# Kernel tuning notes

Hardware: AMD Instinct MI355X
Metric: run time of the kernel (lower is better)

Reference implementation:

```python
import jax, jax.numpy as jnp
import numpy as np

N_NODES = 50000
N_EDGES = 800000
D_FEAT = 128
UNITS = 128


def setup_inputs() -> dict:
    key = jax.random.key(0)
    k1, k2, k3, k4 = jax.random.split(key, 4)
    x = jax.random.normal(k1, (N_NODES, D_FEAT), dtype=jnp.float32)
    source = jax.random.randint(k2, (N_EDGES,), 0, N_NODES, dtype=jnp.int32)
    target = jax.random.randint(k3, (N_EDGES,), 0, N_NODES, dtype=jnp.int32)
    W = jax.random.normal(k4, (D_FEAT, UNITS), dtype=jnp.float32) * (1.0 / np.sqrt(D_FEAT))
    b = jnp.zeros((UNITS,), dtype=jnp.float32)
    return {"x": x, "source": source, "target": target, "W": W, "b": b}


def _degree(idx, n_nodes):
    # in/out degree = segment-sum of unit edge weights; clamp to >= 1 (no self loops)
    deg = jnp.zeros((n_nodes,), dtype=jnp.float32).at[idx].add(1.0)
    return jnp.maximum(deg, 1.0)


def reference(x, source, target, W, b):
    n = x.shape[0]
    # degree_normalization == "in_out": sender scale from out-degree, receiver from in-degree
    sender_scale = jax.lax.rsqrt(_degree(source, n))[:, None]      # [N, 1]
    receiver_scale = jax.lax.rsqrt(_degree(target, n))[:, None]    # [N, 1]
    normalized = sender_scale * x                                  # [N, D]
    source_bcast = normalized[source]                              # [E, D] gather
    pooled = jax.ops.segment_sum(source_bcast, target, num_segments=n)  # [N, D] scatter-add
    pooled = receiver_scale * pooled
    # Dense(units, activation='relu', use_bias=True)
    return jax.nn.relu(pooled @ W + b)
```

## Files before the change

### kernel.cpp

```cpp
#include <hip/hip_runtime.h>
#include <hip/hip_bf16.h>

#define N_FEAT 128
#define EPT 8
#define CHUNK 2048
#define BSHIFT 8
#define MAXRANGE 256
#define CAP 8192
#define LSTR 66

typedef short bf16x8 __attribute__((ext_vector_type(8)));
typedef float f32x4  __attribute__((ext_vector_type(4)));

__device__ __forceinline__ unsigned short f2bf_rtne(float f) {
    unsigned u = __float_as_uint(f);
    u += 0x7fffu + ((u >> 16) & 1u);
    return (unsigned short)(u >> 16);
}
__device__ __forceinline__ float bf2f(unsigned short h) {
    return __uint_as_float((unsigned)h << 16);
}

__global__ __launch_bounds__(256) void scatter_kernel(const int* __restrict__ source,
                                                      const int* __restrict__ target,
                                                      int* __restrict__ curT,
                                                      int* __restrict__ curS,
                                                      unsigned int* __restrict__ pairsT,
                                                      unsigned char* __restrict__ srcB,
                                                      const float* __restrict__ W,
                                                      unsigned short* __restrict__ Whi,
                                                      unsigned short* __restrict__ Wlo,
                                                      int E, int NB, int NBLK) {
    __shared__ unsigned int   lds_pairs[CHUNK];
    __shared__ unsigned short lds_sp[CHUNK];
    __shared__ int ct[MAXRANGE], cs[MAXRANGE];
    __shared__ int st[MAXRANGE], ss[MAXRANGE];
    __shared__ int gt[MAXRANGE], gs[MAXRANGE];
    int tid = threadIdx.x, b = blockIdx.x;

    if (b >= NBLK) {
        int idx = (b - NBLK) * 256 + tid;
        int lane = idx & 63;
        int ks = (idx >> 6) & 3;
        int ct2 = idx >> 8;
        int n  = ct2 * 16 + (lane & 15);
        int k0 = ks * 32 + (lane >> 4) * 8;
        unsigned short h[8], l[8];
        #pragma unroll
        for (int j = 0; j < 8; ++j) {
            float w = W[(k0 + j) * N_FEAT + n];
            unsigned short hh = f2bf_rtne(w);
            h[j] = hh;
            l[j] = f2bf_rtne(w - bf2f(hh));
        }
        size_t off = (size_t)idx * 8;
        *(ushort4*)(Whi + off)     = make_ushort4(h[0], h[1], h[2], h[3]);
        *(ushort4*)(Whi + off + 4) = make_ushort4(h[4], h[5], h[6], h[7]);
        *(ushort4*)(Wlo + off)     = make_ushort4(l[0], l[1], l[2], l[3]);
        *(ushort4*)(Wlo + off + 4) = make_ushort4(l[4], l[5], l[6], l[7]);
        return;
    }

    int base = b * CHUNK;
    int cnt = E - base; if (cnt > CHUNK) cnt = CHUNK;

    int rs[EPT], rt[EPT];
    ct[tid] = 0; cs[tid] = 0;
    __syncthreads();
    #pragma unroll
    for (int j = 0; j < EPT; ++j) {
        int e = base + j * 256 + tid;
        if (e < E) {
            int s = source[e], t = target[e];
            rs[j] = s; rt[j] = t;
            atomicAdd(&ct[t >> BSHIFT], 1);
            atomicAdd(&cs[s >> BSHIFT], 1);
        }
    }
    __syncthreads();
    int vt = ct[tid], vs = cs[tid];
    st[tid] = vt; ss[tid] = vs;
    __syncthreads();
    #pragma unroll
    for (int off = 1; off < 256; off <<= 1) {
        int t1 = (tid >= off) ? st[tid - off] : 0;
        int t2 = (tid >= off) ? ss[tid - off] : 0;
        __syncthreads();
        st[tid] += t1; ss[tid] += t2;
        __syncthreads();
    }
    int et = st[tid] - vt, es = ss[tid] - vs;
    int gT = 0, gS = 0;
    if (tid < NB) {
        if (vt) gT = atomicAdd(&curT[tid], vt);
        if (vs) gS = atomicAdd(&curS[tid], vs);
    }
    __syncthreads();
    st[tid] = et; ss[tid] = es;
    ct[tid] = et; cs[tid] = es;
    gt[tid] = gT; gs[tid] = gS;
    __syncthreads();
    #pragma unroll
    for (int j = 0; j < EPT; ++j) {
        int e = base + j * 256 + tid;
        if (e < E) {
            int s = rs[j], t = rt[j];
            int k = t >> BSHIFT;
            int p = atomicAdd(&ct[k], 1);
            lds_pairs[p] = (unsigned)s | ((unsigned)t << 16);
            int k2 = s >> BSHIFT;
            int p2 = atomicAdd(&cs[k2], 1);
            lds_sp[p2] = (unsigned short)s;
        }
    }
    __syncthreads();
    for (int i = tid; i < cnt; i += 256) {
        unsigned w = lds_pairs[i];
        int k = w >> 24;
        pairsT[(size_t)k * CAP + gt[k] + (i - st[k])] = w;
        unsigned short sp = lds_sp[i];
        int k2 = sp >> 8;
        srcB[(size_t)k2 * CAP + gs[k2] + (i - ss[k2])] = (unsigned char)sp;
    }
}

__global__ __launch_bounds__(256) void prep_kernel(const unsigned char* __restrict__ srcB,
                                                   const unsigned int* __restrict__ pairsT,
                                                   const int* __restrict__ curT,
                                                   const int* __restrict__ curS,
                                                   const float* __restrict__ x,
                                                   const unsigned short* __restrict__ Whi,
                                                   const unsigned short* __restrict__ Wlo,
                                                   unsigned short* __restrict__ Y,
                                                   int2* __restrict__ offs,
                                                   int* __restrict__ elist,
                                                   float* __restrict__ ri,
                                                   int N, int NB) {
    __shared__ int hist[MAXRANGE];
    __shared__ int sb[MAXRANGE];
    __shared__ int excl[MAXRANGE];
    __shared__ int cur[MAXRANGE];
    __shared__ float so_l[MAXRANGE];
    __shared__ unsigned int hi_t[16 * LSTR];
    __shared__ unsigned int lo_t[16 * LSTR];
    int tid = threadIdx.x, b = blockIdx.x;
    int wave = tid >> 6, lane = tid & 63;
    int quad = lane >> 4, k16 = lane & 15;

    if (b < NB) {
        hist[tid] = 0;
        __syncthreads();
        int cnt = curS[b];
        size_t base = (size_t)b * CAP;
        for (int i = tid; i < cnt; i += 256)
            atomicAdd(&hist[srcB[base + i]], 1);
        __syncthreads();
        {
            int d = hist[tid]; if (d < 1) d = 1;
            so_l[tid] = rsqrtf((float)d);
        }
        __syncthreads();
        int row0 = b << BSHIFT;
        int nrows = N - row0; if (nrows > 256) nrows = 256;
        if (nrows <= 0) return;
        const bf16x8* BH = (const bf16x8*)Whi;
        const bf16x8* BL = (const bf16x8*)Wlo;
        for (int t0 = 0; t0 < nrows; t0 += 16) {
            for (int i = tid; i < 1024; i += 256) {
                int r = i >> 6, dw = i & 63;
                int gr = row0 + t0 + r;
                float s = so_l[t0 + r];
                float2 v = make_float2(0.f, 0.f);
                if (gr < N) v = ((const float2*)x)[(size_t)gr * 64 + dw];
                float v0 = s * v.x, v1 = s * v.y;
                unsigned short h0 = f2bf_rtne(v0), h1 = f2bf_rtne(v1);
                unsigned short l0 = f2bf_rtne(v0 - bf2f(h0));
                unsigned short l1 = f2bf_rtne(v1 - bf2f(h1));
                hi_t[r * LSTR + dw] = (unsigned)h0 | ((unsigned)h1 << 16);
                lo_t[r * LSTR + dw] = (unsigned)l0 | ((unsigned)l1 << 16);
            }
            __syncthreads();
            bf16x8 Ahi[4], Alo[4];
            int m = k16;
            #pragma unroll
            for (int ks = 0; ks < 4; ++ks) {
                int a = m * LSTR + ks * 16 + quad * 4;
                Ahi[ks] = *(const bf16x8*)(hi_t + a);
                Alo[ks] = *(const bf16x8*)(lo_t + a);
            }
            #pragma unroll
            for (int c = 0; c < 2; ++c) {
                int ctile = wave * 2 + c;
                f32x4 acc = {0.f, 0.f, 0.f, 0.f};
                #pragma unroll
                for (int ks = 0; ks < 4; ++ks) {
                    bf16x8 bh = BH[(ctile * 4 + ks) * 64 + lane];
                    bf16x8 bl = BL[(ctile * 4 + ks) * 64 + lane];
                    acc = __builtin_amdgcn_mfma_f32_16x16x32_bf16(Ahi[ks], bh, acc, 0, 0, 0);
                    acc = __builtin_amdgcn_mfma_f32_16x16x32_bf16(Alo[ks], bh, acc, 0, 0, 0);
                    acc = __builtin_amdgcn_mfma_f32_16x16x32_bf16(Ahi[ks], bl, acc, 0, 0, 0);
                }
                int colc = ctile * 16 + m;
                #pragma unroll
                for (int reg = 0; reg < 4; ++reg) {
                    int gr = row0 + t0 + quad * 4 + reg;
                    if (gr < N)
                        Y[(size_t)gr * N_FEAT + colc] = f2bf_rtne(acc[reg]);
                }
            }
            __syncthreads();
        }
    } else {
        int bb = b - NB;
        hist[tid] = 0; cur[tid] = 0;
        __syncthreads();
        int cnt = curT[bb];
        int gbase = bb * CAP;
        for (int i = tid; i < cnt; i += 256)
            atomicAdd(&hist[(pairsT[(size_t)gbase + i] >> 16) & 255], 1);
        __syncthreads();
        int deg = hist[tid];
        sb[tid] = deg;
        __syncthreads();
        #pragma unroll
        for (int off = 1; off < 256; off <<= 1) {
            int t = (tid >= off) ? sb[tid - off] : 0;
            __syncthreads();
            sb[tid] += t;
            __syncthreads();
        }
        excl[tid] = sb[tid] - deg;
        __syncthreads();
        int node = (bb << BSHIFT) + tid;
        if (node < N) {
            int st0 = gbase + excl[tid];
            offs[node] = make_int2(st0, st0 + deg);
            int d = deg; if (d < 1) d = 1;
            ri[node] = rsqrtf((float)d);
        }
        for (int i = tid; i < cnt; i += 256) {
            unsigned w = pairsT[(size_t)gbase + i];
            int tl = (w >> 16) & 255;
            int pos = atomicAdd(&cur[tl], 1);
            elist[gbase + excl[tl] + pos] = (int)(w & 0xFFFFu);
        }
    }
}

#define ACC8(u) { acc[0] += __uint_as_float((u).x << 16); \
                  acc[1] += __uint_as_float((u).x & 0xffff0000u); \
                  acc[2] += __uint_as_float((u).y << 16); \
                  acc[3] += __uint_as_float((u).y & 0xffff0000u); \
                  acc[4] += __uint_as_float((u).z << 16); \
                  acc[5] += __uint_as_float((u).z & 0xffff0000u); \
                  acc[6] += __uint_as_float((u).w << 16); \
                  acc[7] += __uint_as_float((u).w & 0xffff0000u); }

__global__ __launch_bounds__(128) void agg_kernel(const unsigned short* __restrict__ Y,
                                                  const int* __restrict__ elist,
                                                  const int2* __restrict__ offs,
                                                  const float* __restrict__ ri,
                                                  const float* __restrict__ bias,
                                                  float* __restrict__ out,
                                                  int N) {
    int tid  = threadIdx.x;
    int wave = tid >> 6, lane = tid & 63;
    int quad = lane >> 4, k16 = lane & 15;
    int node = blockIdx.x * 8 + wave * 4 + quad;
    if (node >= N) return;
    const uint4* yr = (const uint4*)Y;
    int2 oe = offs[node];
    float rr = ri[node];
    float acc[8] = {0.f, 0.f, 0.f, 0.f, 0.f, 0.f, 0.f, 0.f};
    int j = oe.x, je = oe.y;
    for (; j + 8 <= je; j += 8) {
        int e0 = elist[j],     e1 = elist[j + 1];
        int e2 = elist[j + 2], e3 = elist[j + 3];
        int e4 = elist[j + 4], e5 = elist[j + 5];
        int e6 = elist[j + 6], e7 = elist[j + 7];
        uint4 u0 = yr[(size_t)e0 * 16 + k16];
        uint4 u1 = yr[(size_t)e1 * 16 + k16];
        uint4 u2 = yr[(size_t)e2 * 16 + k16];
        uint4 u3 = yr[(size_t)e3 * 16 + k16];
        uint4 u4 = yr[(size_t)e4 * 16 + k16];
        uint4 u5 = yr[(size_t)e5 * 16 + k16];
        uint4 u6 = yr[(size_t)e6 * 16 + k16];
        uint4 u7 = yr[(size_t)e7 * 16 + k16];
        ACC8(u0) ACC8(u1) ACC8(u2) ACC8(u3)
        ACC8(u4) ACC8(u5) ACC8(u6) ACC8(u7)
    }
    for (; j < je; ++j) {
        int e = elist[j];
        uint4 u = yr[(size_t)e * 16 + k16];
        ACC8(u)
    }
    int f0 = k16 * 8;
    const float4* bp = (const float4*)(bias + f0);
    float4 b0 = bp[0], b1 = bp[1];
    float4 o0, o1;
    o0.x = fmaxf(acc[0] * rr + b0.x, 0.f);
    o0.y = fmaxf(acc[1] * rr + b0.y, 0.f);
    o0.z = fmaxf(acc[2] * rr + b0.z, 0.f);
    o0.w = fmaxf(acc[3] * rr + b0.w, 0.f);
    o1.x = fmaxf(acc[4] * rr + b1.x, 0.f);
    o1.y = fmaxf(acc[5] * rr + b1.y, 0.f);
    o1.z = fmaxf(acc[6] * rr + b1.z, 0.f);
    o1.w = fmaxf(acc[7] * rr + b1.w, 0.f);
    float4* op = (float4*)(out + (size_t)node * N_FEAT + f0);
    op[0] = o0;
    op[1] = o1;
}

extern "C" void kernel_launch(void* const* d_in, const int* in_sizes, int n_in,
                              void* d_out, int out_size, void* d_ws, size_t ws_size,
                              hipStream_t stream) {
    const float* x      = (const float*)d_in[0];
    const int*   source = (const int*)d_in[1];
    const int*   target = (const int*)d_in[2];
    const float* W      = (const float*)d_in[3];
    const float* bias   = (const float*)d_in[4];
    float*       out    = (float*)d_out;

    const int N = in_sizes[0] / N_FEAT;
    const int E = in_sizes[1];

    const int NB   = (N + MAXRANGE - 1) >> BSHIFT;
    const int NBLK = (E + CHUNK - 1) / CHUNK;

    uintptr_t p = (uintptr_t)d_ws;
    auto carve = [&](size_t bytes) {
        p = (p + 255) & ~(uintptr_t)255;
        uintptr_t r = p;
        p += bytes;
        return (void*)r;
    };
    int*            curs    = (int*)carve((size_t)2 * NB * sizeof(int));
    int*            curT    = curs;
    int*            curS    = curs + NB;
    unsigned int*   pairsT  = (unsigned int*)carve((size_t)NB * CAP * sizeof(unsigned int));
    int*            elist   = (int*)carve((size_t)NB * CAP * sizeof(int));
    unsigned char*  srcB    = (unsigned char*)carve((size_t)NB * CAP);
    float*          ri      = (float*)carve((size_t)N * sizeof(float));
    int2*           offs    = (int2*)carve((size_t)N * sizeof(int2));
    unsigned short* Y       = (unsigned short*)carve((size_t)N * N_FEAT * sizeof(unsigned short));
    unsigned short* Whi     = (unsigned short*)carve((size_t)N_FEAT * N_FEAT * sizeof(unsigned short));
    unsigned short* Wlo     = (unsigned short*)carve((size_t)N_FEAT * N_FEAT * sizeof(unsigned short));
    (void)ws_size; (void)n_in; (void)out_size;

    (void)hipMemsetAsync(curs, 0, (size_t)2 * NB * sizeof(int), stream);

    scatter_kernel<<<NBLK + 8, 256, 0, stream>>>(source, target, curT, curS, pairsT, srcB,
                                                 W, Whi, Wlo, E, NB, NBLK);
    prep_kernel<<<2 * NB, 256, 0, stream>>>(srcB, pairsT, curT, curS, x, Whi, Wlo,
                                            Y, offs, elist, ri, N, NB);
    agg_kernel<<<(N + 7) / 8, 128, 0, stream>>>(Y, elist, offs, ri, bias, out, N);
}
```

Before: 174.5 us.

## Split feature GEMM out of prep kernel into separate fine-grained kernel

The per-bucket prep blocks previously computed out-degree scales and then ran the whole 256-row x·W GEMM serially in 16-row tiles. Now prep only writes the sender scale to a global array, and a new kernel launches one block per 16 rows to do the split-bf16 MFMA GEMM. This spreads the GEMM over far more blocks (about 3125 instead of about 196) to improve occupancy across CUs, at the cost of an extra launch and a global round-trip for the scale array.

```diff
diff --git a/kernel.cpp b/kernel.cpp
--- a/kernel.cpp
+++ b/kernel.cpp
@@ -128,10 +128,7 @@
                                                    const unsigned int* __restrict__ pairsT,
                                                    const int* __restrict__ curT,
                                                    const int* __restrict__ curS,
-                                                   const float* __restrict__ x,
-                                                   const unsigned short* __restrict__ Whi,
-                                                   const unsigned short* __restrict__ Wlo,
-                                                   unsigned short* __restrict__ Y,
+                                                   float* __restrict__ so,
                                                    int2* __restrict__ offs,
                                                    int* __restrict__ elist,
                                                    float* __restrict__ ri,
@@ -140,12 +137,7 @@
     __shared__ int sb[MAXRANGE];
     __shared__ int excl[MAXRANGE];
     __shared__ int cur[MAXRANGE];
-    __shared__ float so_l[MAXRANGE];
-    __shared__ unsigned int hi_t[16 * LSTR];
-    __shared__ unsigned int lo_t[16 * LSTR];
     int tid = threadIdx.x, b = blockIdx.x;
-    int wave = tid >> 6, lane = tid & 63;
-    int quad = lane >> 4, k16 = lane & 15;
 
     if (b < NB) {
         hist[tid] = 0;
@@ -155,60 +147,10 @@
         for (int i = tid; i < cnt; i += 256)
             atomicAdd(&hist[srcB[base + i]], 1);
         __syncthreads();
-        {
+        int node = (b << BSHIFT) + tid;
+        if (node < N) {
             int d = hist[tid]; if (d < 1) d = 1;
-            so_l[tid] = rsqrtf((float)d);
-        }
-        __syncthreads();
-        int row0 = b << BSHIFT;
-        int nrows = N - row0; if (nrows > 256) nrows = 256;
-        if (nrows <= 0) return;
-        const bf16x8* BH = (const bf16x8*)Whi;
-        const bf16x8* BL = (const bf16x8*)Wlo;
-        for (int t0 = 0; t0 < nrows; t0 += 16) {
-            for (int i = tid; i < 1024; i += 256) {
-                int r = i >> 6, dw = i & 63;
-                int gr = row0 + t0 + r;
-                float s = so_l[t0 + r];
-                float2 v = make_float2(0.f, 0.f);
-                if (gr < N) v = ((const float2*)x)[(size_t)gr * 64 + dw];
-                float v0 = s * v.x, v1 = s * v.y;
-                unsigned short h0 = f2bf_rtne(v0), h1 = f2bf_rtne(v1);
-                unsigned short l0 = f2bf_rtne(v0 - bf2f(h0));
-                unsigned short l1 = f2bf_rtne(v1 - bf2f(h1));
-                hi_t[r * LSTR + dw] = (unsigned)h0 | ((unsigned)h1 << 16);
-                lo_t[r * LSTR + dw] = (unsigned)l0 | ((unsigned)l1 << 16);
-            }
-            __syncthreads();
-            bf16x8 Ahi[4], Alo[4];
-            int m = k16;
-            #pragma unroll
-            for (int ks = 0; ks < 4; ++ks) {
-                int a = m * LSTR + ks * 16 + quad * 4;
-                Ahi[ks] = *(const bf16x8*)(hi_t + a);
-                Alo[ks] = *(const bf16x8*)(lo_t + a);
-            }
-            #pragma unroll
-            for (int c = 0; c < 2; ++c) {
-                int ctile = wave * 2 + c;
-                f32x4 acc = {0.f, 0.f, 0.f, 0.f};
-                #pragma unroll
-                for (int ks = 0; ks < 4; ++ks) {
-                    bf16x8 bh = BH[(ctile * 4 + ks) * 64 + lane];
-                    bf16x8 bl = BL[(ctile * 4 + ks) * 64 + lane];
-                    acc = __builtin_amdgcn_mfma_f32_16x16x32_bf16(Ahi[ks], bh, acc, 0, 0, 0);
-                    acc = __builtin_amdgcn_mfma_f32_16x16x32_bf16(Alo[ks], bh, acc, 0, 0, 0);
-                    acc = __builtin_amdgcn_mfma_f32_16x16x32_bf16(Ahi[ks], bl, acc, 0, 0, 0);
-                }
-                int colc = ctile * 16 + m;
-                #pragma unroll
-                for (int reg = 0; reg < 4; ++reg) {
-                    int gr = row0 + t0 + quad * 4 + reg;
-                    if (gr < N)
-                        Y[(size_t)gr * N_FEAT + colc] = f2bf_rtne(acc[reg]);
-                }
-            }
-            __syncthreads();
+            so[node] = rsqrtf((float)d);
         }
     } else {
         int bb = b - NB;
@@ -243,6 +185,69 @@
             int tl = (w >> 16) & 255;
             int pos = atomicAdd(&cur[tl], 1);
             elist[gbase + excl[tl] + pos] = (int)(w & 0xFFFFu);
+        }
+    }
+}
+
+__global__ __launch_bounds__(256) void ygemm_kernel(const float* __restrict__ x,
+                                                    const float* __restrict__ so,
+                                                    const unsigned short* __restrict__ Whi,
+                                                    const unsigned short* __restrict__ Wlo,
+                                                    unsigned short* __restrict__ Y,
+                                                    int N) {
+    __shared__ unsigned int hi_t[16 * LSTR];
+    __shared__ unsigned int lo_t[16 * LSTR];
+    int tid = threadIdx.x;
+    int wave = tid >> 6, lane = tid & 63;
+    int quad = lane >> 4, k16 = lane & 15;
+    int row0 = blockIdx.x * 16;
+
+    for (int i = tid; i < 1024; i += 256) {
+        int r = i >> 6, dw = i & 63;
+        int gr = row0 + r;
+        float2 v = make_float2(0.f, 0.f);
+        float s = 0.f;
+        if (gr < N) {
+            v = ((const float2*)x)[(size_t)gr * 64 + dw];
+            s = so[gr];
+        }
+        float v0 = s * v.x, v1 = s * v.y;
+        unsigned short h0 = f2bf_rtne(v0), h1 = f2bf_rtne(v1);
+        unsigned short l0 = f2bf_rtne(v0 - bf2f(h0));
+        unsigned short l1 = f2bf_rtne(v1 - bf2f(h1));
+        hi_t[r * LSTR + dw] = (unsigned)h0 | ((unsigned)h1 << 16);
+        lo_t[r * LSTR + dw] = (unsigned)l0 | ((unsigned)l1 << 16);
+    }
+    __syncthreads();
+
+    bf16x8 Ahi[4], Alo[4];
+    int m = k16;
+    #pragma unroll
+    for (int ks = 0; ks < 4; ++ks) {
+        int a = m * LSTR + ks * 16 + quad * 4;
+        Ahi[ks] = *(const bf16x8*)(hi_t + a);
+        Alo[ks] = *(const bf16x8*)(lo_t + a);
+    }
+    const bf16x8* BH = (const bf16x8*)Whi;
+    const bf16x8* BL = (const bf16x8*)Wlo;
+    #pragma unroll
+    for (int c = 0; c < 2; ++c) {
+        int ctile = wave * 2 + c;
+        f32x4 acc = {0.f, 0.f, 0.f, 0.f};
+        #pragma unroll
+        for (int ks = 0; ks < 4; ++ks) {
+            bf16x8 bh = BH[(ctile * 4 + ks) * 64 + lane];
+            bf16x8 bl = BL[(ctile * 4 + ks) * 64 + lane];
+            acc = __builtin_amdgcn_mfma_f32_16x16x32_bf16(Ahi[ks], bh, acc, 0, 0, 0);
+            acc = __builtin_amdgcn_mfma_f32_16x16x32_bf16(Alo[ks], bh, acc, 0, 0, 0);
+            acc = __builtin_amdgcn_mfma_f32_16x16x32_bf16(Ahi[ks], bl, acc, 0, 0, 0);
+        }
+        int colc = ctile * 16 + m;
+        #pragma unroll
+        for (int reg = 0; reg < 4; ++reg) {
+            int gr = row0 + quad * 4 + reg;
+            if (gr < N)
+                Y[(size_t)gr * N_FEAT + colc] = f2bf_rtne(acc[reg]);
         }
     }
 }
@@ -341,6 +346,7 @@
     int*            elist   = (int*)carve((size_t)NB * CAP * sizeof(int));
     unsigned char*  srcB    = (unsigned char*)carve((size_t)NB * CAP);
     float*          ri      = (float*)carve((size_t)N * sizeof(float));
+    float*          so      = (float*)carve((size_t)N * sizeof(float));
     int2*           offs    = (int2*)carve((size_t)N * sizeof(int2));
     unsigned short* Y       = (unsigned short*)carve((size_t)N * N_FEAT * sizeof(unsigned short));
     unsigned short* Whi     = (unsigned short*)carve((size_t)N_FEAT * N_FEAT * sizeof(unsigned short));
@@ -351,7 +357,8 @@
 
     scatter_kernel<<<NBLK + 8, 256, 0, stream>>>(source, target, curT, curS, pairsT, srcB,
                                                  W, Whi, Wlo, E, NB, NBLK);
-    prep_kernel<<<2 * NB, 256, 0, stream>>>(srcB, pairsT, curT, curS, x, Whi, Wlo,
-                                            Y, offs, elist, ri, N, NB);
+    prep_kernel<<<2 * NB, 256, 0, stream>>>(srcB, pairsT, curT, curS, so,
+                                            offs, elist, ri, N, NB);
+    ygemm_kernel<<<(N + 15) / 16, 256, 0, stream>>>(x, so, Whi, Wlo, Y, N);
     agg_kernel<<<(N + 7) / 8, 128, 0, stream>>>(Y, elist, offs, ri, bias, out, N);
 }
```

After: 159.1 us. 8.8% less time.
